# Kernel tuning notes

Measured on AMD Instinct MI355X. Metric: run time of the kernel, lower is better.

The kernel has to match this reference:

```python
import jax, jax.numpy as jnp
import numpy as np

DIM_MODEL = 1024
DIM_K = 64
DIM_V = 64
H = 16
B = 2
S = 2048


def setup_inputs() -> dict:
    key = jax.random.key(0)
    ks = jax.random.split(key, 11)
    s = 0.02
    return {
        "Q": jax.random.normal(ks[0], (B, S, DIM_MODEL), jnp.float32),
        "K": jax.random.normal(ks[1], (B, S, DIM_MODEL), jnp.float32),
        "V": jax.random.normal(ks[2], (B, S, DIM_MODEL), jnp.float32),
        "Wq": jax.random.normal(ks[3], (DIM_MODEL, H * DIM_K), jnp.float32) * s,
        "bq": jnp.zeros((H * DIM_K,), jnp.float32),
        "Wk": jax.random.normal(ks[4], (DIM_MODEL, H * DIM_K), jnp.float32) * s,
        "bk": jnp.zeros((H * DIM_K,), jnp.float32),
        "Wv": jax.random.normal(ks[5], (DIM_MODEL, H * DIM_V), jnp.float32) * s,
        "bv": jnp.zeros((H * DIM_V,), jnp.float32),
        "Wo": jax.random.normal(ks[6], (H * DIM_V, DIM_MODEL), jnp.float32) * s,
        "bo": jnp.zeros((DIM_MODEL,), jnp.float32),
    }


def reference(Q, K, V, Wq, bq, Wk, bk, Wv, bv, Wo, bo):
    b, len_q = Q.shape[0], Q.shape[1]
    # QKV projections, split heads: [b, h, S, d]
    q = (Q @ Wq + bq).reshape(b, len_q, H, DIM_K).transpose(0, 2, 1, 3)
    k = (K @ Wk + bk).reshape(b, K.shape[1], H, DIM_K).transpose(0, 2, 1, 3)
    v = (V @ Wv + bv).reshape(b, V.shape[1], H, DIM_V).transpose(0, 2, 1, 3)
    # FAITHFUL QUIRK: original scales by sqrt(K.shape[0]) == batch size, not dim_k
    scale = 1.0 / np.sqrt(b).astype(np.float32)
    att = jnp.einsum('bhqd,bhkd->bhqk', q * scale, k)
    att = jax.nn.softmax(att, axis=-1)
    out = jnp.einsum('bhqk,bhkd->bhqd', att, v)  # [b,h,S,dv]
    out = out.transpose(0, 2, 1, 3).reshape(b, len_q, H * DIM_V)
    return out @ Wo + bo
```

## Files before the change

### kernel.cpp

```cpp
#include <hip/hip_runtime.h>
#include <hip/hip_bf16.h>


using bf16 = __hip_bfloat16;
typedef __attribute__((ext_vector_type(4))) float f32x4;
typedef __attribute__((ext_vector_type(8))) short bf16x8;

__device__ __forceinline__ void gload_lds16(const void* gsrc, void* ldst) {
    __builtin_amdgcn_global_load_lds(
        (const __attribute__((address_space(1))) void*)gsrc,
        (__attribute__((address_space(3))) void*)ldst,
        16, 0, 0);
}

__device__ __forceinline__ float fexp2(float x) {
    float r; asm("v_exp_f32 %0, %1" : "=v"(r) : "v"(x)); return r;
}

__device__ __forceinline__ unsigned cvtpk(float a, float b) {
    unsigned d; asm("v_cvt_pk_bf16_f32 %0, %1, %2" : "=v"(d) : "v"(a), "v"(b));
    return d;
}

__device__ __forceinline__ void pls32(unsigned &a, unsigned &b) {
    asm("v_permlane32_swap_b32 %0, %1" : "+v"(a), "+v"(b));
}
__device__ __forceinline__ void pls16(unsigned &a, unsigned &b) {
    asm("v_permlane16_swap_b32 %0, %1" : "+v"(a), "+v"(b));
}

__device__ __forceinline__ unsigned pack2bf(float a, float b) {
    unsigned short ua = __builtin_bit_cast(unsigned short, __float2bfloat16(a));
    unsigned short ub = __builtin_bit_cast(unsigned short, __float2bfloat16(b));
    return (unsigned)ua | ((unsigned)ub << 16);
}

__global__ void conv3_kernel(const float* __restrict__ X0, const float* __restrict__ X1,
                             const float* __restrict__ X2,
                             bf16* __restrict__ O0, bf16* __restrict__ O1, bf16* __restrict__ O2,
                             int n4) {
    int z = blockIdx.z;
    const float* in = z == 0 ? X0 : (z == 1 ? X1 : X2);
    bf16* out = z == 0 ? O0 : (z == 1 ? O1 : O2);
    int idx = blockIdx.x * blockDim.x + threadIdx.x;
    int stride = gridDim.x * blockDim.x;
    for (int i = idx; i < n4; i += stride) {
        float4 v = reinterpret_cast<const float4*>(in)[i];
        reinterpret_cast<uint2*>(out)[i] = make_uint2(pack2bf(v.x, v.y), pack2bf(v.z, v.w));
    }
}

__global__ void transpose4_kernel(const float* __restrict__ W0, const float* __restrict__ W1,
                                  const float* __restrict__ W2, const float* __restrict__ W3,
                                  bf16* __restrict__ T0, bf16* __restrict__ T1,
                                  bf16* __restrict__ T2, bf16* __restrict__ T3) {
    int z = blockIdx.z;
    const float* W = z == 0 ? W0 : (z == 1 ? W1 : (z == 2 ? W2 : W3));
    bf16* WT = z == 0 ? T0 : (z == 1 ? T1 : (z == 2 ? T2 : T3));
    __shared__ float t[32][33];
    int bx = blockIdx.x * 32, by = blockIdx.y * 32;
    int x = threadIdx.x, y = threadIdx.y;
    #pragma unroll
    for (int i = 0; i < 4; ++i)
        t[y + 8*i][x] = W[(size_t)(by + y + 8*i) * 1024 + bx + x];
    __syncthreads();
    #pragma unroll
    for (int i = 0; i < 4; ++i)
        WT[(size_t)(bx + y + 8*i) * 1024 + by + x] = __float2bfloat16(t[x][y + 8*i]);
}

template<int NTILE>
__global__ __launch_bounds__(256, 3)
void gemm_bt(const bf16* __restrict__ A0, const bf16* __restrict__ A1, const bf16* __restrict__ A2,
             const bf16* __restrict__ B0, const bf16* __restrict__ B1, const bf16* __restrict__ B2,
             const float* __restrict__ bi0, const float* __restrict__ bi1, const float* __restrict__ bi2,
             void* __restrict__ O0, void* __restrict__ O1, void* __restrict__ O2,
             int mode_base)
{
    const int f = blockIdx.x;
    int x, y, z;
    if (NTILE == 128) {
        const int s = f >> 3;
        y = s & 7;
        const int t = (f & 7) + 8 * (s >> 3);
        x = t & 31; z = t >> 5;
    } else {
        const int s = f >> 3;
        y = s & 15;
        x = (f & 7) + 8 * (s >> 4);
        z = 0;
    }
    const bf16* A  = z == 0 ? A0 : (z == 1 ? A1 : A2);
    const bf16* BT = z == 0 ? B0 : (z == 1 ? B1 : B2);
    const float* bias = z == 0 ? bi0 : (z == 1 ? bi1 : bi2);
    void* Cout = z == 0 ? O0 : (z == 1 ? O1 : O2);
    const int mode = mode_base + z;

    constexpr int MF = (NTILE == 128) ? 4 : 2;
    __shared__ __align__(16) char Abuf[16384];
    __shared__ __align__(16) char Bbuf[NTILE * 128];
    const int tid = threadIdx.x;
    const int wave = tid >> 6, lane = tid & 63;
    const int g = lane >> 4, ln = lane & 15;
    const int m0 = x * 128, n0 = y * NTILE;
    const int wm = (NTILE == 128) ? (wave >> 1) * 64 : wave * 32;
    const int wn = (NTILE == 128) ? (wave & 1) * 64 : 0;
    const int lnsw = (ln & 7) << 4;

    f32x4 acc[MF][4] = {};

    for (int k0 = 0; k0 < 1024; k0 += 64) {
        __syncthreads();
        #pragma unroll
        for (int rd = 0; rd < 4; ++rd) {
            int row = rd * 32 + (tid >> 3);
            int src = ((tid & 7) * 16) ^ (((tid >> 3) & 7) << 4);
            gload_lds16((const char*)(A + (size_t)(m0 + row) * 1024 + k0) + src,
                        Abuf + rd * 4096 + tid * 16);
        }
        #pragma unroll
        for (int rd = 0; rd < NTILE / 32; ++rd) {
            int row = rd * 32 + (tid >> 3);
            int src = ((tid & 7) * 16) ^ (((tid >> 3) & 7) << 4);
            gload_lds16((const char*)(BT + (size_t)(n0 + row) * 1024 + k0) + src,
                        Bbuf + rd * 4096 + tid * 16);
        }
        __syncthreads();
        #pragma unroll
        for (int kk = 0; kk < 2; ++kk) {
            bf16x8 af[MF], bfr[4];
            #pragma unroll
            for (int mf = 0; mf < MF; ++mf)
                af[mf] = *(const bf16x8*)&Abuf[(wm + mf*16 + ln) * 128 + ((kk*64 + g*16) ^ lnsw)];
            #pragma unroll
            for (int nf = 0; nf < 4; ++nf)
                bfr[nf] = *(const bf16x8*)&Bbuf[(wn + nf*16 + ln) * 128 + ((kk*64 + g*16) ^ lnsw)];
            #pragma unroll
            for (int mf = 0; mf < MF; ++mf)
                #pragma unroll
                for (int nf = 0; nf < 4; ++nf)
                    acc[mf][nf] = __builtin_amdgcn_mfma_f32_16x16x32_bf16(af[mf], bfr[nf], acc[mf][nf], 0, 0, 0);
        }
    }

    const float scl = (mode == 0) ? (0.70710678118654752f * 1.44269504088896340f) : 1.0f;
    #pragma unroll
    for (int mf = 0; mf < MF; ++mf) {
        #pragma unroll
        for (int nf = 0; nf < 4; ++nf) {
            int col = n0 + wn + nf*16 + ln;
            float bv = bias[col];
            #pragma unroll
            for (int r = 0; r < 4; ++r) {
                int row = m0 + wm + mf*16 + g*4 + r;
                float v = (acc[mf][nf][r] + bv) * scl;
                if (mode == 0 || mode == 1) {
                    ((bf16*)Cout)[(size_t)row * 1024 + col] = __float2bfloat16(v);
                } else if (mode == 2) {
                    int b = row >> 11, ss = row & 2047;
                    int hh = col >> 6, dv = col & 63;
                    ((bf16*)Cout)[(((size_t)(b*16 + hh) * 64 + dv) << 11) + ss] = __float2bfloat16(v);
                } else {
                    ((float*)Cout)[(size_t)row * 1024 + col] = v;
                }
            }
        }
    }
}

__global__ __launch_bounds__(256, 2)
void attn_kernel(const bf16* __restrict__ qh, const bf16* __restrict__ kh,
                 const bf16* __restrict__ vt, bf16* __restrict__ aout)
{
    __shared__ __align__(16) bf16 Kls[2][64 * 64];
    __shared__ __align__(16) bf16 Vls[2][64 * 64];
    const int f = blockIdx.x;
    const int xcd = f & 7, s = f >> 3, i = s & 15, ghi = s >> 4;
    const int bh = xcd + 8 * ghi;
    const int b = bh >> 4, h = bh & 15;
    const int q0 = i * 128;

    const int tid = threadIdx.x;
    const int wave = tid >> 6, lane = tid & 63;
    const int g = lane >> 4, ln = lane & 15;
    const int srow = lane >> 3;
    const int scol = ((lane & 7) * 16) ^ ((srow & 7) << 4);
    const int lnsw = (ln & 7) << 4;

    const bf16* kbase = kh + (size_t)(b * 2048) * 1024 + h * 64;
    const bf16* vbase = vt + (size_t)bh * 64 * 2048;

    bf16x8 qf[2][2];
    #pragma unroll
    for (int nf = 0; nf < 2; ++nf) {
        const bf16* qrow = qh + (size_t)(b*2048 + q0 + wave*32 + nf*16 + ln) * 1024 + h*64;
        qf[nf][0] = *(const bf16x8*)(qrow + g*8);
        qf[nf][1] = *(const bf16x8*)(qrow + 32 + g*8);
    }

    #pragma unroll
    for (int c2 = 0; c2 < 2; ++c2) {
        int c = wave * 2 + c2;
        int row = c * 8 + srow;
        gload_lds16((const char*)(kbase + (size_t)row * 1024) + scol, (char*)&Kls[0][0] + c * 1024);
        gload_lds16((const char*)(vbase + (size_t)row * 2048) + scol, (char*)&Vls[0][0] + c * 1024);
    }

    f32x4 oacc[4][2] = {};
    float lsum[2] = {0.f, 0.f};
    union PU { unsigned u[4]; bf16x8 v; };

    for (int t = 0; t < 32; ++t) {
        const int cur = t & 1;
        if (t < 31) {
            const int kv0n = (t + 1) * 64;
            #pragma unroll
            for (int c2 = 0; c2 < 2; ++c2) {
                int c = wave * 2 + c2;
                int row = c * 8 + srow;
                gload_lds16((const char*)(kbase + (size_t)(kv0n + row) * 1024) + scol,
                            (char*)&Kls[cur ^ 1][0] + c * 1024);
                gload_lds16((const char*)(vbase + (size_t)row * 2048 + kv0n) + scol,
                            (char*)&Vls[cur ^ 1][0] + c * 1024);
            }
            asm volatile("s_waitcnt vmcnt(4)\n\ts_barrier" ::: "memory");
        } else {
            asm volatile("s_waitcnt vmcnt(0)\n\ts_barrier" ::: "memory");
        }
        __builtin_amdgcn_sched_barrier(0);

        const char* Kc = (const char*)&Kls[cur][0];
        const char* Vc = (const char*)&Vls[cur][0];

        f32x4 sac[4][2] = {};
        __builtin_amdgcn_s_setprio(1);
        #pragma unroll
        for (int kk = 0; kk < 2; ++kk) {
            bf16x8 kf[4];
            #pragma unroll
            for (int mf = 0; mf < 4; ++mf)
                kf[mf] = *(const bf16x8*)(Kc + (mf*16 + ln) * 128 + ((kk*64 + g*16) ^ lnsw));
            #pragma unroll
            for (int mf = 0; mf < 4; ++mf)
                #pragma unroll
                for (int nf = 0; nf < 2; ++nf)
                    sac[mf][nf] = __builtin_amdgcn_mfma_f32_16x16x32_bf16(kf[mf], qf[nf][kk], sac[mf][nf], 0, 0, 0);
        }
        __builtin_amdgcn_s_setprio(0);

        PU pf[2][2];
        #pragma unroll
        for (int nf = 0; nf < 2; ++nf) {
            unsigned w[4][2];
            #pragma unroll
            for (int mf = 0; mf < 4; ++mf) {
                float e0 = fexp2(sac[mf][nf][0]);
                float e1 = fexp2(sac[mf][nf][1]);
                float e2 = fexp2(sac[mf][nf][2]);
                float e3 = fexp2(sac[mf][nf][3]);
                lsum[nf] += (e0 + e1) + (e2 + e3);
                w[mf][0] = cvtpk(e0, e1);
                w[mf][1] = cvtpk(e2, e3);
            }
            #pragma unroll
            for (int kk = 0; kk < 2; ++kk) {
                #pragma unroll
                for (int rp = 0; rp < 2; ++rp) {
                    unsigned a = w[2*kk][rp], bb = w[2*kk + 1][rp];
                    pls32(a, bb);
                    pls16(a, bb);
                    pf[nf][kk].u[rp] = a;
                    pf[nf][kk].u[2 + rp] = bb;
                }
            }
        }

        __builtin_amdgcn_s_setprio(1);
        #pragma unroll
        for (int kk = 0; kk < 2; ++kk) {
            bf16x8 vf[4];
            #pragma unroll
            for (int mf = 0; mf < 4; ++mf)
                vf[mf] = *(const bf16x8*)(Vc + (mf*16 + ln) * 128 + ((kk*64 + g*16) ^ lnsw));
            #pragma unroll
            for (int mf = 0; mf < 4; ++mf)
                #pragma unroll
                for (int nf = 0; nf < 2; ++nf)
                    oacc[mf][nf] = __builtin_amdgcn_mfma_f32_16x16x32_bf16(vf[mf], pf[nf][kk].v, oacc[mf][nf], 0, 0, 0);
        }
        __builtin_amdgcn_s_setprio(0);
        __builtin_amdgcn_sched_barrier(0);
        asm volatile("s_barrier" ::: "memory");
    }

    #pragma unroll
    for (int nf = 0; nf < 2; ++nf) {
        float l = lsum[nf];
        l += __shfl_xor(l, 16);
        l += __shfl_xor(l, 32);
        float inv = 1.0f / l;
        int q = q0 + wave*32 + nf*16 + ln;
        bf16* orow = aout + (size_t)(b*2048 + q) * 1024 + h * 64;
        #pragma unroll
        for (int mf = 0; mf < 4; ++mf) {
            *(uint2*)(orow + mf*16 + g*4) = make_uint2(
                pack2bf(oacc[mf][nf][0] * inv, oacc[mf][nf][1] * inv),
                pack2bf(oacc[mf][nf][2] * inv, oacc[mf][nf][3] * inv));
        }
    }
}

extern "C" void kernel_launch(void* const* d_in, const int* in_sizes, int n_in,
                              void* d_out, int out_size, void* d_ws, size_t ws_size,
                              hipStream_t stream)
{
    const float* Q  = (const float*)d_in[0];
    const float* K  = (const float*)d_in[1];
    const float* V  = (const float*)d_in[2];
    const float* Wq = (const float*)d_in[3];
    const float* bq = (const float*)d_in[4];
    const float* Wk = (const float*)d_in[5];
    const float* bk = (const float*)d_in[6];
    const float* Wv = (const float*)d_in[7];
    const float* bv = (const float*)d_in[8];
    const float* Wo = (const float*)d_in[9];
    const float* bo = (const float*)d_in[10];

    char* ws = (char*)d_ws;
    const size_t MB = 1024 * 1024;
    bf16* Qbf  = (bf16*)(ws + 0);
    bf16* Kbf  = (bf16*)(ws + 8*MB);
    bf16* Vbf  = (bf16*)(ws + 16*MB);
    bf16* WqT  = (bf16*)(ws + 24*MB);
    bf16* WkT  = (bf16*)(ws + 26*MB);
    bf16* WvT  = (bf16*)(ws + 28*MB);
    bf16* WoT  = (bf16*)(ws + 30*MB);
    bf16* qhp  = (bf16*)(ws + 32*MB);
    bf16* khp  = (bf16*)(ws + 40*MB);
    bf16* vtp  = (bf16*)(ws + 48*MB);
    bf16* aout = (bf16*)(ws + 0);

    const int n4 = (2 * 2048 * 1024) / 4;
    conv3_kernel<<<dim3(512, 1, 3), 256, 0, stream>>>(Q, K, V, Qbf, Kbf, Vbf, n4);

    transpose4_kernel<<<dim3(32, 32, 4), dim3(32, 8), 0, stream>>>(Wq, Wk, Wv, Wo, WqT, WkT, WvT, WoT);

    gemm_bt<128><<<768, 256, 0, stream>>>(Qbf, Kbf, Vbf, WqT, WkT, WvT,
                                          bq, bk, bv, qhp, khp, vtp, 0);

    attn_kernel<<<512, 256, 0, stream>>>(qhp, khp, vtp, aout);

    gemm_bt<64><<<512, 256, 0, stream>>>(aout, aout, aout, WoT, WoT, WoT,
                                         bo, bo, bo, d_out, d_out, d_out, 3);
}
```

Baseline: 119.8 us.

## Double KV tile to 128 and compute softmax row sums via MFMA with ones

Each attention pipeline iteration now stages 128 keys/values instead of 64 into LDS, halving the number of barrier-synchronised steps and changing the V tile swizzle to match the wider row. The per-lane fp32 accumulation of exp values, plus the final cross-lane shuffle reduction, is replaced by an extra MFMA that multiplies the bf16 probability fragments by a ones vector. This cuts VALU work and sync overhead. In exchange it doubles LDS use, which may lower occupancy, and the row sum is now computed from bf16-rounded probabilities.

```diff
diff --git a/kernel.cpp b/kernel.cpp
--- a/kernel.cpp
+++ b/kernel.cpp
@@ -172,8 +172,8 @@
 void attn_kernel(const bf16* __restrict__ qh, const bf16* __restrict__ kh,
                  const bf16* __restrict__ vt, bf16* __restrict__ aout)
 {
-    __shared__ __align__(16) bf16 Kls[2][64 * 64];
-    __shared__ __align__(16) bf16 Vls[2][64 * 64];
+    __shared__ __align__(16) bf16 Kls[2][128 * 64];
+    __shared__ __align__(16) bf16 Vls[2][64 * 128];
     const int f = blockIdx.x;
     const int xcd = f & 7, s = f >> 3, i = s & 15, ghi = s >> 4;
     const int bh = xcd + 8 * ghi;
@@ -190,6 +190,9 @@
     const bf16* kbase = kh + (size_t)(b * 2048) * 1024 + h * 64;
     const bf16* vbase = vt + (size_t)bh * 64 * 2048;
 
+    const int vrow_in = lane >> 4;
+    const int vcol16 = lane & 15;
+
     bf16x8 qf[2][2];
     #pragma unroll
     for (int nf = 0; nf < 2; ++nf) {
@@ -198,32 +201,37 @@
         qf[nf][1] = *(const bf16x8*)(qrow + 32 + g*8);
     }
 
-    #pragma unroll
-    for (int c2 = 0; c2 < 2; ++c2) {
-        int c = wave * 2 + c2;
-        int row = c * 8 + srow;
-        gload_lds16((const char*)(kbase + (size_t)row * 1024) + scol, (char*)&Kls[0][0] + c * 1024);
-        gload_lds16((const char*)(vbase + (size_t)row * 2048) + scol, (char*)&Vls[0][0] + c * 1024);
-    }
+    auto stageKV = [&](int kv0, int buf) {
+        #pragma unroll
+        for (int c2 = 0; c2 < 4; ++c2) {
+            int c = wave * 4 + c2;
+            int krow = c * 8 + srow;
+            gload_lds16((const char*)(kbase + (size_t)(kv0 + krow) * 1024) + scol,
+                        (char*)&Kls[buf][0] + c * 1024);
+        }
+        #pragma unroll
+        for (int c2 = 0; c2 < 4; ++c2) {
+            int c = wave * 4 + c2;
+            int vrow = c * 4 + vrow_in;
+            int sc16 = vcol16 ^ (vrow & 15);
+            gload_lds16((const char*)(vbase + (size_t)vrow * 2048 + kv0) + sc16 * 16,
+                        (char*)&Vls[buf][0] + c * 1024);
+        }
+    };
+
+    stageKV(0, 0);
 
     f32x4 oacc[4][2] = {};
-    float lsum[2] = {0.f, 0.f};
+    f32x4 lacc[2] = {};
     union PU { unsigned u[4]; bf16x8 v; };
-
-    for (int t = 0; t < 32; ++t) {
+    PU ones;
+    ones.u[0] = ones.u[1] = ones.u[2] = ones.u[3] = 0x3F803F80u;
+
+    for (int t = 0; t < 16; ++t) {
         const int cur = t & 1;
-        if (t < 31) {
-            const int kv0n = (t + 1) * 64;
-            #pragma unroll
-            for (int c2 = 0; c2 < 2; ++c2) {
-                int c = wave * 2 + c2;
-                int row = c * 8 + srow;
-                gload_lds16((const char*)(kbase + (size_t)(kv0n + row) * 1024) + scol,
-                            (char*)&Kls[cur ^ 1][0] + c * 1024);
-                gload_lds16((const char*)(vbase + (size_t)row * 2048 + kv0n) + scol,
-                            (char*)&Vls[cur ^ 1][0] + c * 1024);
-            }
-            asm volatile("s_waitcnt vmcnt(4)\n\ts_barrier" ::: "memory");
+        if (t < 15) {
+            stageKV((t + 1) * 128, cur ^ 1);
+            asm volatile("s_waitcnt vmcnt(8)\n\ts_barrier" ::: "memory");
         } else {
             asm volatile("s_waitcnt vmcnt(0)\n\ts_barrier" ::: "memory");
         }
@@ -232,7 +240,7 @@
         const char* Kc = (const char*)&Kls[cur][0];
         const char* Vc = (const char*)&Vls[cur][0];
 
-        f32x4 sac[4][2] = {};
+        f32x4 sacA[4][2] = {}, sacB[4][2] = {};
         __builtin_amdgcn_s_setprio(1);
         #pragma unroll
         for (int kk = 0; kk < 2; ++kk) {
@@ -244,61 +252,75 @@
             for (int mf = 0; mf < 4; ++mf)
                 #pragma unroll
                 for (int nf = 0; nf < 2; ++nf)
-                    sac[mf][nf] = __builtin_amdgcn_mfma_f32_16x16x32_bf16(kf[mf], qf[nf][kk], sac[mf][nf], 0, 0, 0);
+                    sacA[mf][nf] = __builtin_amdgcn_mfma_f32_16x16x32_bf16(kf[mf], qf[nf][kk], sacA[mf][nf], 0, 0, 0);
+        }
+        #pragma unroll
+        for (int kk = 0; kk < 2; ++kk) {
+            bf16x8 kf[4];
+            #pragma unroll
+            for (int mf = 0; mf < 4; ++mf)
+                kf[mf] = *(const bf16x8*)(Kc + (64 + mf*16 + ln) * 128 + ((kk*64 + g*16) ^ lnsw));
+            #pragma unroll
+            for (int mf = 0; mf < 4; ++mf)
+                #pragma unroll
+                for (int nf = 0; nf < 2; ++nf)
+                    sacB[mf][nf] = __builtin_amdgcn_mfma_f32_16x16x32_bf16(kf[mf], qf[nf][kk], sacB[mf][nf], 0, 0, 0);
         }
         __builtin_amdgcn_s_setprio(0);
 
-        PU pf[2][2];
-        #pragma unroll
-        for (int nf = 0; nf < 2; ++nf) {
-            unsigned w[4][2];
-            #pragma unroll
-            for (int mf = 0; mf < 4; ++mf) {
-                float e0 = fexp2(sac[mf][nf][0]);
-                float e1 = fexp2(sac[mf][nf][1]);
-                float e2 = fexp2(sac[mf][nf][2]);
-                float e3 = fexp2(sac[mf][nf][3]);
-                lsum[nf] += (e0 + e1) + (e2 + e3);
-                w[mf][0] = cvtpk(e0, e1);
-                w[mf][1] = cvtpk(e2, e3);
-            }
-            #pragma unroll
-            for (int kk = 0; kk < 2; ++kk) {
-                #pragma unroll
-                for (int rp = 0; rp < 2; ++rp) {
-                    unsigned a = w[2*kk][rp], bb = w[2*kk + 1][rp];
-                    pls32(a, bb);
-                    pls16(a, bb);
-                    pf[nf][kk].u[rp] = a;
-                    pf[nf][kk].u[2 + rp] = bb;
+        #pragma unroll
+        for (int ha = 0; ha < 2; ++ha) {
+            f32x4 (&sac)[4][2] = ha ? sacB : sacA;
+            PU pf[2][2];
+            #pragma unroll
+            for (int nf = 0; nf < 2; ++nf) {
+                unsigned w[4][2];
+                #pragma unroll
+                for (int mf = 0; mf < 4; ++mf) {
+                    float e0 = fexp2(sac[mf][nf][0]);
+                    float e1 = fexp2(sac[mf][nf][1]);
+                    float e2 = fexp2(sac[mf][nf][2]);
+                    float e3 = fexp2(sac[mf][nf][3]);
+                    w[mf][0] = cvtpk(e0, e1);
+                    w[mf][1] = cvtpk(e2, e3);
+                }
+                #pragma unroll
+                for (int kk = 0; kk < 2; ++kk) {
+                    #pragma unroll
+                    for (int rp = 0; rp < 2; ++rp) {
+                        unsigned a = w[2*kk][rp], bb = w[2*kk + 1][rp];
+                        pls32(a, bb);
+                        pls16(a, bb);
+                        pf[nf][kk].u[rp] = a;
+                        pf[nf][kk].u[2 + rp] = bb;
+                    }
                 }
             }
-        }
-
-        __builtin_amdgcn_s_setprio(1);
-        #pragma unroll
-        for (int kk = 0; kk < 2; ++kk) {
-            bf16x8 vf[4];
-            #pragma unroll
-            for (int mf = 0; mf < 4; ++mf)
-                vf[mf] = *(const bf16x8*)(Vc + (mf*16 + ln) * 128 + ((kk*64 + g*16) ^ lnsw));
-            #pragma unroll
-            for (int mf = 0; mf < 4; ++mf)
+            __builtin_amdgcn_s_setprio(1);
+            #pragma unroll
+            for (int kk = 0; kk < 2; ++kk) {
+                bf16x8 vf[4];
+                #pragma unroll
+                for (int mf = 0; mf < 4; ++mf)
+                    vf[mf] = *(const bf16x8*)(Vc + (mf*16 + ln) * 256 + (((ha*8 + kk*4 + g) ^ ln) << 4));
                 #pragma unroll
                 for (int nf = 0; nf < 2; ++nf)
-                    oacc[mf][nf] = __builtin_amdgcn_mfma_f32_16x16x32_bf16(vf[mf], pf[nf][kk].v, oacc[mf][nf], 0, 0, 0);
-        }
-        __builtin_amdgcn_s_setprio(0);
+                    lacc[nf] = __builtin_amdgcn_mfma_f32_16x16x32_bf16(ones.v, pf[nf][kk].v, lacc[nf], 0, 0, 0);
+                #pragma unroll
+                for (int mf = 0; mf < 4; ++mf)
+                    #pragma unroll
+                    for (int nf = 0; nf < 2; ++nf)
+                        oacc[mf][nf] = __builtin_amdgcn_mfma_f32_16x16x32_bf16(vf[mf], pf[nf][kk].v, oacc[mf][nf], 0, 0, 0);
+            }
+            __builtin_amdgcn_s_setprio(0);
+        }
         __builtin_amdgcn_sched_barrier(0);
         asm volatile("s_barrier" ::: "memory");
     }
 
     #pragma unroll
     for (int nf = 0; nf < 2; ++nf) {
-        float l = lsum[nf];
-        l += __shfl_xor(l, 16);
-        l += __shfl_xor(l, 32);
-        float inv = 1.0f / l;
+        float inv = 1.0f / lacc[nf][0];
         int q = q0 + wave*32 + nf*16 + ln;
         bf16* orow = aout + (size_t)(b*2048 + q) * 1024 + h * 64;
         #pragma unroll
```

Measured after the change: 115.4 us. -3.7%, faster.

## Split attention KV range across two blocks and merge with combine kernel

Applied to the files above, without the earlier changes.

The attention kernel now splits each query tile's KV sequence into two halves, launching twice as many blocks with higher occupancy bounds. Each block writes unnormalized partial outputs in bf16 plus row sums, and a new combine kernel adds the halves and normalizes. Row sums are now computed on the matrix cores by multiplying a ones vector with the probabilities, replacing scalar adds. This adds an extra kernel launch, extra global traffic and bf16 rounding of the partial outputs.

```diff
diff --git a/kernel.cpp b/kernel.cpp
--- a/kernel.cpp
+++ b/kernel.cpp
@@ -33,6 +33,10 @@
     unsigned short ua = __builtin_bit_cast(unsigned short, __float2bfloat16(a));
     unsigned short ub = __builtin_bit_cast(unsigned short, __float2bfloat16(b));
     return (unsigned)ua | ((unsigned)ub << 16);
+}
+
+__device__ __forceinline__ float bfu(unsigned lo16) {
+    return __builtin_bit_cast(float, lo16 << 16);
 }
 
 __global__ void conv3_kernel(const float* __restrict__ X0, const float* __restrict__ X1,
@@ -168,17 +172,20 @@
     }
 }
 
-__global__ __launch_bounds__(256, 2)
+__global__ __launch_bounds__(256, 4)
 void attn_kernel(const bf16* __restrict__ qh, const bf16* __restrict__ kh,
-                 const bf16* __restrict__ vt, bf16* __restrict__ aout)
+                 const bf16* __restrict__ vt, bf16* __restrict__ Opart,
+                 float* __restrict__ lpart)
 {
     __shared__ __align__(16) bf16 Kls[2][64 * 64];
     __shared__ __align__(16) bf16 Vls[2][64 * 64];
     const int f = blockIdx.x;
-    const int xcd = f & 7, s = f >> 3, i = s & 15, ghi = s >> 4;
+    const int xcd = f & 7, r = f >> 3, j = r & 31, ghi = r >> 5;
     const int bh = xcd + 8 * ghi;
     const int b = bh >> 4, h = bh & 15;
+    const int i = j >> 1, half = j & 1;
     const int q0 = i * 128;
+    const int kvbase = half * 1024;
 
     const int tid = threadIdx.x;
     const int wave = tid >> 6, lane = tid & 63;
@@ -198,31 +205,30 @@
         qf[nf][1] = *(const bf16x8*)(qrow + 32 + g*8);
     }
 
-    #pragma unroll
-    for (int c2 = 0; c2 < 2; ++c2) {
-        int c = wave * 2 + c2;
-        int row = c * 8 + srow;
-        gload_lds16((const char*)(kbase + (size_t)row * 1024) + scol, (char*)&Kls[0][0] + c * 1024);
-        gload_lds16((const char*)(vbase + (size_t)row * 2048) + scol, (char*)&Vls[0][0] + c * 1024);
-    }
+    auto stageKV = [&](int kv0, int buf) {
+        #pragma unroll
+        for (int c2 = 0; c2 < 2; ++c2) {
+            int c = wave * 2 + c2;
+            int row = c * 8 + srow;
+            gload_lds16((const char*)(kbase + (size_t)(kv0 + row) * 1024) + scol,
+                        (char*)&Kls[buf][0] + c * 1024);
+            gload_lds16((const char*)(vbase + (size_t)row * 2048 + kv0) + scol,
+                        (char*)&Vls[buf][0] + c * 1024);
+        }
+    };
+
+    stageKV(kvbase, 0);
 
     f32x4 oacc[4][2] = {};
-    float lsum[2] = {0.f, 0.f};
+    f32x4 lacc[2] = {};
     union PU { unsigned u[4]; bf16x8 v; };
-
-    for (int t = 0; t < 32; ++t) {
+    PU ones;
+    ones.u[0] = ones.u[1] = ones.u[2] = ones.u[3] = 0x3F803F80u;
+
+    for (int t = 0; t < 16; ++t) {
         const int cur = t & 1;
-        if (t < 31) {
-            const int kv0n = (t + 1) * 64;
-            #pragma unroll
-            for (int c2 = 0; c2 < 2; ++c2) {
-                int c = wave * 2 + c2;
-                int row = c * 8 + srow;
-                gload_lds16((const char*)(kbase + (size_t)(kv0n + row) * 1024) + scol,
-                            (char*)&Kls[cur ^ 1][0] + c * 1024);
-                gload_lds16((const char*)(vbase + (size_t)row * 2048 + kv0n) + scol,
-                            (char*)&Vls[cur ^ 1][0] + c * 1024);
-            }
+        if (t < 15) {
+            stageKV(kvbase + (t + 1) * 64, cur ^ 1);
             asm volatile("s_waitcnt vmcnt(4)\n\ts_barrier" ::: "memory");
         } else {
             asm volatile("s_waitcnt vmcnt(0)\n\ts_barrier" ::: "memory");
@@ -258,7 +264,6 @@
                 float e1 = fexp2(sac[mf][nf][1]);
                 float e2 = fexp2(sac[mf][nf][2]);
                 float e3 = fexp2(sac[mf][nf][3]);
-                lsum[nf] += (e0 + e1) + (e2 + e3);
                 w[mf][0] = cvtpk(e0, e1);
                 w[mf][1] = cvtpk(e2, e3);
             }
@@ -283,6 +288,9 @@
             for (int mf = 0; mf < 4; ++mf)
                 vf[mf] = *(const bf16x8*)(Vc + (mf*16 + ln) * 128 + ((kk*64 + g*16) ^ lnsw));
             #pragma unroll
+            for (int nf = 0; nf < 2; ++nf)
+                lacc[nf] = __builtin_amdgcn_mfma_f32_16x16x32_bf16(ones.v, pf[nf][kk].v, lacc[nf], 0, 0, 0);
+            #pragma unroll
             for (int mf = 0; mf < 4; ++mf)
                 #pragma unroll
                 for (int nf = 0; nf < 2; ++nf)
@@ -293,21 +301,45 @@
         asm volatile("s_barrier" ::: "memory");
     }
 
+    bf16* Oh = Opart + (size_t)half * 4096 * 1024;
+    float* lh = lpart + (size_t)half * 4096 * 16;
     #pragma unroll
     for (int nf = 0; nf < 2; ++nf) {
-        float l = lsum[nf];
-        l += __shfl_xor(l, 16);
-        l += __shfl_xor(l, 32);
-        float inv = 1.0f / l;
         int q = q0 + wave*32 + nf*16 + ln;
-        bf16* orow = aout + (size_t)(b*2048 + q) * 1024 + h * 64;
+        int row = b*2048 + q;
+        if (g == 0) lh[row * 16 + h] = lacc[nf][0];
+        bf16* orow = Oh + (size_t)row * 1024 + h * 64;
         #pragma unroll
         for (int mf = 0; mf < 4; ++mf) {
             *(uint2*)(orow + mf*16 + g*4) = make_uint2(
-                pack2bf(oacc[mf][nf][0] * inv, oacc[mf][nf][1] * inv),
-                pack2bf(oacc[mf][nf][2] * inv, oacc[mf][nf][3] * inv));
-        }
-    }
+                pack2bf(oacc[mf][nf][0], oacc[mf][nf][1]),
+                pack2bf(oacc[mf][nf][2], oacc[mf][nf][3]));
+        }
+    }
+}
+
+__global__ void combine_kernel(const unsigned short* __restrict__ Op,
+                               const float* __restrict__ lpart,
+                               bf16* __restrict__ aout)
+{
+    int idx = blockIdx.x * blockDim.x + threadIdx.x;
+    if (idx >= 4096 * 128) return;
+    int q = idx >> 7, c = idx & 127;
+    int h = c >> 3;
+    float inv = 1.0f / (lpart[q * 16 + h] + lpart[65536 + q * 16 + h]);
+    const uint4 a = *(const uint4*)(Op + (size_t)q * 1024 + c * 8);
+    const uint4 b = *(const uint4*)(Op + (size_t)(4096 + q) * 1024 + c * 8);
+    unsigned o[4];
+    const unsigned* ap = &a.x;
+    const unsigned* bp = &b.x;
+    #pragma unroll
+    for (int w = 0; w < 4; ++w) {
+        float lo = bfu(ap[w] & 0xffffu) + bfu(bp[w] & 0xffffu);
+        float hi = __builtin_bit_cast(float, ap[w] & 0xffff0000u)
+                 + __builtin_bit_cast(float, bp[w] & 0xffff0000u);
+        o[w] = pack2bf(lo * inv, hi * inv);
+    }
+    *(uint4*)(aout + (size_t)q * 1024 + c * 8) = make_uint4(o[0], o[1], o[2], o[3]);
 }
 
 extern "C" void kernel_launch(void* const* d_in, const int* in_sizes, int n_in,
@@ -328,17 +360,19 @@
 
     char* ws = (char*)d_ws;
     const size_t MB = 1024 * 1024;
-    bf16* Qbf  = (bf16*)(ws + 0);
-    bf16* Kbf  = (bf16*)(ws + 8*MB);
-    bf16* Vbf  = (bf16*)(ws + 16*MB);
-    bf16* WqT  = (bf16*)(ws + 24*MB);
-    bf16* WkT  = (bf16*)(ws + 26*MB);
-    bf16* WvT  = (bf16*)(ws + 28*MB);
-    bf16* WoT  = (bf16*)(ws + 30*MB);
-    bf16* qhp  = (bf16*)(ws + 32*MB);
-    bf16* khp  = (bf16*)(ws + 40*MB);
-    bf16* vtp  = (bf16*)(ws + 48*MB);
-    bf16* aout = (bf16*)(ws + 0);
+    bf16* Qbf   = (bf16*)(ws + 0);
+    bf16* Kbf   = (bf16*)(ws + 8*MB);
+    bf16* Vbf   = (bf16*)(ws + 16*MB);
+    bf16* WqT   = (bf16*)(ws + 24*MB);
+    bf16* WkT   = (bf16*)(ws + 26*MB);
+    bf16* WvT   = (bf16*)(ws + 28*MB);
+    bf16* WoT   = (bf16*)(ws + 30*MB);
+    bf16* qhp   = (bf16*)(ws + 32*MB);
+    bf16* khp   = (bf16*)(ws + 40*MB);
+    bf16* vtp   = (bf16*)(ws + 48*MB);
+    bf16* Opart = (bf16*)(ws + 0);
+    float* lpart = (float*)(ws + 16*MB);
+    bf16* aout  = (bf16*)(ws + 17*MB);
 
     const int n4 = (2 * 2048 * 1024) / 4;
     conv3_kernel<<<dim3(512, 1, 3), 256, 0, stream>>>(Q, K, V, Qbf, Kbf, Vbf, n4);
@@ -348,7 +382,9 @@
     gemm_bt<128><<<768, 256, 0, stream>>>(Qbf, Kbf, Vbf, WqT, WkT, WvT,
                                           bq, bk, bv, qhp, khp, vtp, 0);
 
-    attn_kernel<<<512, 256, 0, stream>>>(qhp, khp, vtp, aout);
+    attn_kernel<<<1024, 256, 0, stream>>>(qhp, khp, vtp, Opart, lpart);
+
+    combine_kernel<<<2048, 256, 0, stream>>>((const unsigned short*)Opart, lpart, aout);
 
     gemm_bt<64><<<512, 256, 0, stream>>>(aout, aout, aout, WoT, WoT, WoT,
                                          bo, bo, bo, d_out, d_out, d_out, 3);
```

Measured after the change: 121.2 us. No clear change (+1.1%).

## Software-pipeline QK^T with previous tile's softmax-PV; compute row sums via MFMA

Applied to the files above, without the earlier changes.

Restructures the attention loop so the QK^T MFMAs for tile t are issued before the exp/PV work for tile t-1, with a triple-buffered V LDS ring and two alternating score register sets. This lets MFMA work overlap the exp and pack VALU work. The softmax denominator is now accumulated with an extra MFMA against a ones vector instead of VALU adds and cross-lane shuffles. The cost is higher register pressure from the two score sets and extra LDS for the third V buffer.

```diff
diff --git a/kernel.cpp b/kernel.cpp
--- a/kernel.cpp
+++ b/kernel.cpp
@@ -173,7 +173,7 @@
                  const bf16* __restrict__ vt, bf16* __restrict__ aout)
 {
     __shared__ __align__(16) bf16 Kls[2][64 * 64];
-    __shared__ __align__(16) bf16 Vls[2][64 * 64];
+    __shared__ __align__(16) bf16 Vls[3][64 * 64];
     const int f = blockIdx.x;
     const int xcd = f & 7, s = f >> 3, i = s & 15, ghi = s >> 4;
     const int bh = xcd + 8 * ghi;
@@ -189,6 +189,8 @@
 
     const bf16* kbase = kh + (size_t)(b * 2048) * 1024 + h * 64;
     const bf16* vbase = vt + (size_t)bh * 64 * 2048;
+    char* Kb = (char*)&Kls[0][0];
+    char* Vb = (char*)&Vls[0][0];
 
     bf16x8 qf[2][2];
     #pragma unroll
@@ -198,56 +200,28 @@
         qf[nf][1] = *(const bf16x8*)(qrow + 32 + g*8);
     }
 
-    #pragma unroll
-    for (int c2 = 0; c2 < 2; ++c2) {
-        int c = wave * 2 + c2;
-        int row = c * 8 + srow;
-        gload_lds16((const char*)(kbase + (size_t)row * 1024) + scol, (char*)&Kls[0][0] + c * 1024);
-        gload_lds16((const char*)(vbase + (size_t)row * 2048) + scol, (char*)&Vls[0][0] + c * 1024);
-    }
+    auto stageKV = [&](int kv0, int kbuf, int vbuf) {
+        #pragma unroll
+        for (int c2 = 0; c2 < 2; ++c2) {
+            int c = wave * 2 + c2;
+            int row = c * 8 + srow;
+            gload_lds16((const char*)(kbase + (size_t)(kv0 + row) * 1024) + scol,
+                        Kb + kbuf * 8192 + c * 1024);
+            gload_lds16((const char*)(vbase + (size_t)row * 2048 + kv0) + scol,
+                        Vb + vbuf * 8192 + c * 1024);
+        }
+    };
 
     f32x4 oacc[4][2] = {};
-    float lsum[2] = {0.f, 0.f};
+    f32x4 lacc[2] = {};
+    f32x4 sacA[4][2], sacB[4][2];
     union PU { unsigned u[4]; bf16x8 v; };
-
-    for (int t = 0; t < 32; ++t) {
-        const int cur = t & 1;
-        if (t < 31) {
-            const int kv0n = (t + 1) * 64;
-            #pragma unroll
-            for (int c2 = 0; c2 < 2; ++c2) {
-                int c = wave * 2 + c2;
-                int row = c * 8 + srow;
-                gload_lds16((const char*)(kbase + (size_t)(kv0n + row) * 1024) + scol,
-                            (char*)&Kls[cur ^ 1][0] + c * 1024);
-                gload_lds16((const char*)(vbase + (size_t)row * 2048 + kv0n) + scol,
-                            (char*)&Vls[cur ^ 1][0] + c * 1024);
-            }
-            asm volatile("s_waitcnt vmcnt(4)\n\ts_barrier" ::: "memory");
-        } else {
-            asm volatile("s_waitcnt vmcnt(0)\n\ts_barrier" ::: "memory");
-        }
-        __builtin_amdgcn_sched_barrier(0);
-
-        const char* Kc = (const char*)&Kls[cur][0];
-        const char* Vc = (const char*)&Vls[cur][0];
-
-        f32x4 sac[4][2] = {};
-        __builtin_amdgcn_s_setprio(1);
-        #pragma unroll
-        for (int kk = 0; kk < 2; ++kk) {
-            bf16x8 kf[4];
-            #pragma unroll
-            for (int mf = 0; mf < 4; ++mf)
-                kf[mf] = *(const bf16x8*)(Kc + (mf*16 + ln) * 128 + ((kk*64 + g*16) ^ lnsw));
-            #pragma unroll
-            for (int mf = 0; mf < 4; ++mf)
-                #pragma unroll
-                for (int nf = 0; nf < 2; ++nf)
-                    sac[mf][nf] = __builtin_amdgcn_mfma_f32_16x16x32_bf16(kf[mf], qf[nf][kk], sac[mf][nf], 0, 0, 0);
-        }
-        __builtin_amdgcn_s_setprio(0);
-
+    PU ones;
+    ones.u[0] = ones.u[1] = ones.u[2] = ones.u[3] = 0x3F803F80u;
+
+    int vS = 1, vC = 0, vP = 2;
+
+    auto SMPV = [&](f32x4 (&sac)[4][2], int vbuf) {
         PU pf[2][2];
         #pragma unroll
         for (int nf = 0; nf < 2; ++nf) {
@@ -258,7 +232,6 @@
                 float e1 = fexp2(sac[mf][nf][1]);
                 float e2 = fexp2(sac[mf][nf][2]);
                 float e3 = fexp2(sac[mf][nf][3]);
-                lsum[nf] += (e0 + e1) + (e2 + e3);
                 w[mf][0] = cvtpk(e0, e1);
                 w[mf][1] = cvtpk(e2, e3);
             }
@@ -274,7 +247,7 @@
                 }
             }
         }
-
+        const char* Vc = Vb + vbuf * 8192;
         __builtin_amdgcn_s_setprio(1);
         #pragma unroll
         for (int kk = 0; kk < 2; ++kk) {
@@ -282,6 +255,9 @@
             #pragma unroll
             for (int mf = 0; mf < 4; ++mf)
                 vf[mf] = *(const bf16x8*)(Vc + (mf*16 + ln) * 128 + ((kk*64 + g*16) ^ lnsw));
+            #pragma unroll
+            for (int nf = 0; nf < 2; ++nf)
+                lacc[nf] = __builtin_amdgcn_mfma_f32_16x16x32_bf16(ones.v, pf[nf][kk].v, lacc[nf], 0, 0, 0);
             #pragma unroll
             for (int mf = 0; mf < 4; ++mf)
                 #pragma unroll
@@ -289,16 +265,59 @@
                     oacc[mf][nf] = __builtin_amdgcn_mfma_f32_16x16x32_bf16(vf[mf], pf[nf][kk].v, oacc[mf][nf], 0, 0, 0);
         }
         __builtin_amdgcn_s_setprio(0);
+    };
+
+    auto iter = [&](int t, f32x4 (&sacNew)[4][2], f32x4 (&sacOld)[4][2], bool doPrev) {
+        if (t < 31) {
+            stageKV((t + 1) * 64, (t + 1) & 1, vS);
+            asm volatile("s_waitcnt vmcnt(4)\n\ts_barrier" ::: "memory");
+        } else {
+            asm volatile("s_waitcnt vmcnt(0)\n\ts_barrier" ::: "memory");
+        }
         __builtin_amdgcn_sched_barrier(0);
-        asm volatile("s_barrier" ::: "memory");
-    }
+
+        const char* Kc = Kb + (t & 1) * 8192;
+        #pragma unroll
+        for (int mf = 0; mf < 4; ++mf)
+            #pragma unroll
+            for (int nf = 0; nf < 2; ++nf)
+                sacNew[mf][nf] = f32x4{0.f, 0.f, 0.f, 0.f};
+        __builtin_amdgcn_s_setprio(1);
+        #pragma unroll
+        for (int kk = 0; kk < 2; ++kk) {
+            bf16x8 kf[4];
+            #pragma unroll
+            for (int mf = 0; mf < 4; ++mf)
+                kf[mf] = *(const bf16x8*)(Kc + (mf*16 + ln) * 128 + ((kk*64 + g*16) ^ lnsw));
+            #pragma unroll
+            for (int mf = 0; mf < 4; ++mf)
+                #pragma unroll
+                for (int nf = 0; nf < 2; ++nf)
+                    sacNew[mf][nf] = __builtin_amdgcn_mfma_f32_16x16x32_bf16(kf[mf], qf[nf][kk], sacNew[mf][nf], 0, 0, 0);
+        }
+        __builtin_amdgcn_s_setprio(0);
+        __builtin_amdgcn_sched_barrier(0);
+
+        if (doPrev)
+            SMPV(sacOld, vP);
+
+        asm volatile("s_waitcnt lgkmcnt(0)\n\ts_barrier" ::: "memory");
+        int t0 = vP; (void)t0;
+        vP = vC; vC = vS; vS = (vS == 2) ? 0 : vS + 1;
+    };
+
+    stageKV(0, 0, 0);
+    iter(0, sacA, sacB, false);
+    for (int p = 0; p < 15; ++p) {
+        iter(2 * p + 1, sacB, sacA, true);
+        iter(2 * p + 2, sacA, sacB, true);
+    }
+    iter(31, sacB, sacA, true);
+    SMPV(sacB, vP);
 
     #pragma unroll
     for (int nf = 0; nf < 2; ++nf) {
-        float l = lsum[nf];
-        l += __shfl_xor(l, 16);
-        l += __shfl_xor(l, 32);
-        float inv = 1.0f / l;
+        float inv = 1.0f / lacc[nf][0];
         int q = q0 + wave*32 + nf*16 + ln;
         bf16* orow = aout + (size_t)(b*2048 + q) * 1024 + h * 64;
         #pragma unroll
```

Result: faster. 117.2 us (-2.2%).
